# Optimization experiments

Hardware: AMD Instinct MI355X
Metric: run time of the kernel (lower is better)

The kernel has to match this reference:

```python
import jax, jax.numpy as jnp
import numpy as np

HIDDEN = 2048
NUM_INPUTS = 4
ACTIVE_IDX = 0
EPS = 1e-6


def rms_norm(x, scale, eps=EPS):
    # Gemma3n RMSNorm: compute in float32, scale by learned per-channel weight.
    x32 = x.astype(jnp.float32)
    inv = jax.lax.rsqrt(jnp.mean(x32 * x32, axis=-1, keepdims=True) + eps)
    return (x32 * inv * scale.astype(jnp.float32)).astype(x.dtype)


def compute_modalities(x, router_norm_scale, router_w):
    # router_norm -> * hidden_size**-1 -> Dense(N) -> tanh (in fp32)
    router_inputs = rms_norm(x, router_norm_scale) * (1.0 / HIDDEN)
    routed = jnp.einsum('bsh,hn->bsn', router_inputs, router_w)
    return jnp.tanh(routed.astype(jnp.float32)).astype(x.dtype)


def setup_inputs() -> dict:
    key = jax.random.key(0)
    k = jax.random.split(key, 7)
    N, B, S, H = NUM_INPUTS, 4, 2048, HIDDEN
    return {
        'hidden_states': jax.random.normal(k[0], (N, B, S, H), dtype=jnp.float32),
        'activated': jax.random.normal(k[1], (B, S, H), dtype=jnp.float32),
        'router_norm_scale': jnp.ones((H,), dtype=jnp.float32) + 0.02 * jax.random.normal(k[2], (H,), dtype=jnp.float32),
        'router_w': 0.02 * jax.random.normal(k[3], (H, N), dtype=jnp.float32),
        'pred_w': 0.02 * jax.random.normal(k[4], (N, N * N), dtype=jnp.float32),
        'corr_w': 0.02 * jax.random.normal(k[5], (N, N), dtype=jnp.float32),
        'correct_output_scale': jax.random.normal(k[6], (H,), dtype=jnp.float32),
    }


def reference(hidden_states, activated, router_norm_scale, router_w, pred_w, corr_w, correct_output_scale):
    N = NUM_INPUTS
    B, S, H = activated.shape

    # ---- predict ----
    mod_p = compute_modalities(hidden_states[ACTIVE_IDX], router_norm_scale, router_w)  # [B,S,N]
    raw = jnp.einsum('bsn,nk->bsk', mod_p, pred_w).reshape(B, S, N, N)  # [B,S,N,N]
    # keras: transpose(raw,(0,1,3,2)) then matmul(hs^(1,2,3,0), .) then transpose back
    # predictions[m,b,s,h] = sum_n hs[n,b,s,h] * raw[b,s,m,n]
    predictions = jnp.einsum('nbsh,bsmn->mbsh', hidden_states, raw) + hidden_states

    # ---- correct ----
    mod_c = compute_modalities(activated, router_norm_scale, router_w)  # [B,S,N]
    innovation = activated - predictions[ACTIVE_IDX]  # [B,S,H]
    coefs = jnp.einsum('bsn,nm->bsm', mod_c, corr_w) + 1.0  # [B,S,N]
    corrected = predictions + innovation[None] * jnp.transpose(coefs, (2, 0, 1))[..., None]

    # ---- scale_corrected_output ----
    return corrected * correct_output_scale
```

## Files before the change

### kernel.cpp

```cpp
#include <hip/hip_runtime.h>

#define HID 2048
#define NTHREADS 256

typedef float f32x4 __attribute__((ext_vector_type(4)));

__global__ __launch_bounds__(NTHREADS) void altup_fused(
    const float* __restrict__ hs,
    const float* __restrict__ act,
    const float* __restrict__ rns,
    const float* __restrict__ rw,
    const float* __restrict__ pw,
    const float* __restrict__ cw,
    const float* __restrict__ cscale,
    float* __restrict__ out,
    int T)
{
    const int t   = blockIdx.x;
    const int tid = threadIdx.x;
    const int c0  = tid * 4;
    const int c1  = c0 + 1024;

    __shared__ float s_red[4][10];

    const size_t tok     = (size_t)t * HID;
    const size_t strideN = (size_t)T * HID;

    float x0a[4], x0b[4], aa[4], ab[4], nsa[4], nsb[4], wa[16], wb[16];
    *(f32x4*)x0a = *(const f32x4*)(hs  + tok + c0);
    *(f32x4*)x0b = *(const f32x4*)(hs  + tok + c1);
    *(f32x4*)aa  = *(const f32x4*)(act + tok + c0);
    *(f32x4*)ab  = *(const f32x4*)(act + tok + c1);
    *(f32x4*)nsa = *(const f32x4*)(rns + c0);
    *(f32x4*)nsb = *(const f32x4*)(rns + c1);
    #pragma unroll
    for (int r = 0; r < 4; ++r) {
        *(f32x4*)(wa + 4 * r) = *(const f32x4*)(rw + (size_t)(c0 + r) * 4);
        *(f32x4*)(wb + 4 * r) = *(const f32x4*)(rw + (size_t)(c1 + r) * 4);
    }

    float red[10];
    #pragma unroll
    for (int k = 0; k < 10; ++k) red[k] = 0.f;
    #pragma unroll
    for (int j = 0; j < 4; ++j) {
        float x0 = x0a[j], a = aa[j], ns = nsa[j];
        red[0] += x0 * x0;
        red[1] += a * a;
        float xs = x0 * ns, as_ = a * ns;
        #pragma unroll
        for (int n = 0; n < 4; ++n) {
            red[2 + n] += xs  * wa[4 * j + n];
            red[6 + n] += as_ * wa[4 * j + n];
        }
    }
    #pragma unroll
    for (int j = 0; j < 4; ++j) {
        float x0 = x0b[j], a = ab[j], ns = nsb[j];
        red[0] += x0 * x0;
        red[1] += a * a;
        float xs = x0 * ns, as_ = a * ns;
        #pragma unroll
        for (int n = 0; n < 4; ++n) {
            red[2 + n] += xs  * wb[4 * j + n];
            red[6 + n] += as_ * wb[4 * j + n];
        }
    }

    float x1a[4], x1b[4], x2a[4], x2b[4], x3a[4], x3b[4], csa[4], csb[4];
    *(f32x4*)x1a = *(const f32x4*)(hs + 1 * strideN + tok + c0);
    *(f32x4*)x1b = *(const f32x4*)(hs + 1 * strideN + tok + c1);
    *(f32x4*)x2a = *(const f32x4*)(hs + 2 * strideN + tok + c0);
    *(f32x4*)x2b = *(const f32x4*)(hs + 2 * strideN + tok + c1);
    *(f32x4*)x3a = *(const f32x4*)(hs + 3 * strideN + tok + c0);
    *(f32x4*)x3b = *(const f32x4*)(hs + 3 * strideN + tok + c1);
    *(f32x4*)csa = *(const f32x4*)(cscale + c0);
    *(f32x4*)csb = *(const f32x4*)(cscale + c1);

    #pragma unroll
    for (int off = 32; off > 0; off >>= 1) {
        #pragma unroll
        for (int k = 0; k < 10; ++k) red[k] += __shfl_down(red[k], off, 64);
    }
    const int wave = tid >> 6, lane = tid & 63;
    if (lane == 0) {
        #pragma unroll
        for (int k = 0; k < 10; ++k) s_red[wave][k] = red[k];
    }
    __syncthreads();

    float acc[10];
    #pragma unroll
    for (int k = 0; k < 10; ++k)
        acc[k] = s_red[0][k] + s_red[1][k] + s_red[2][k] + s_red[3][k];

    const float invH  = 1.0f / (float)HID;
    const float inv_p = rsqrtf(acc[0] * invH + 1e-6f) * invH;
    const float inv_c = rsqrtf(acc[1] * invH + 1e-6f) * invH;
    float mp[4], mc[4];
    #pragma unroll
    for (int n = 0; n < 4; ++n) {
        mp[n] = tanhf(acc[2 + n] * inv_p);
        mc[n] = tanhf(acc[6 + n] * inv_c);
    }
    float raw[16];
    #pragma unroll
    for (int kk = 0; kk < 16; ++kk)
        raw[kk] = mp[0] * pw[kk]      + mp[1] * pw[16 + kk]
                + mp[2] * pw[32 + kk] + mp[3] * pw[48 + kk];
    float coef[4];
    #pragma unroll
    for (int m = 0; m < 4; ++m)
        coef[m] = 1.0f + mc[0] * cw[m]     + mc[1] * cw[4 + m]
                       + mc[2] * cw[8 + m] + mc[3] * cw[12 + m];

    auto emit = [&](const float* x0, const float* x1, const float* x2,
                    const float* x3, const float* a, const float* cs,
                    size_t off) {
        float o[4][4];
        #pragma unroll
        for (int j = 0; j < 4; ++j) {
            float x[4] = { x0[j], x1[j], x2[j], x3[j] };
            float pred[4];
            #pragma unroll
            for (int m = 0; m < 4; ++m)
                pred[m] = x[0] * raw[4 * m + 0] + x[1] * raw[4 * m + 1]
                        + x[2] * raw[4 * m + 2] + x[3] * raw[4 * m + 3] + x[m];
            float innov = a[j] - pred[0];
            #pragma unroll
            for (int m = 0; m < 4; ++m)
                o[m][j] = (pred[m] + innov * coef[m]) * cs[j];
        }
        #pragma unroll
        for (int m = 0; m < 4; ++m)
            __builtin_nontemporal_store(*(const f32x4*)o[m],
                                        (f32x4*)(out + (size_t)m * strideN + off));
    };
    emit(x0a, x1a, x2a, x3a, aa, csa, tok + c0);
    emit(x0b, x1b, x2b, x3b, ab, csb, tok + c1);
}

extern "C" void kernel_launch(void* const* d_in, const int* in_sizes, int n_in,
                              void* d_out, int out_size, void* d_ws, size_t ws_size,
                              hipStream_t stream) {
    const float* hs  = (const float*)d_in[0];
    const float* act = (const float*)d_in[1];
    const float* rns = (const float*)d_in[2];
    const float* rw  = (const float*)d_in[3];
    const float* pw  = (const float*)d_in[4];
    const float* cw  = (const float*)d_in[5];
    const float* cs  = (const float*)d_in[6];
    float* out = (float*)d_out;

    const int T = in_sizes[1] / HID;
    altup_fused<<<dim3(T), dim3(NTHREADS), 0, stream>>>(hs, act, rns, rw, pw, cw, cs, out, T);
}
```

Before: 492.0 us.

## Assign one token per wavefront and drop block-level shared-memory reduction

Each 64-lane wave now processes a whole token (8 chunks of 256 columns), so the reduction is done purely with xor-shuffles and the shared-memory staging and __syncthreads are gone. The grid shrinks by four because each block handles four tokens. The second pass reloads hidden_states slot 0 and the activated row from memory (likely L2) instead of keeping them in registers, which trades extra cache traffic for lower register pressure and no block barrier.

```diff
diff --git a/kernel.cpp b/kernel.cpp
--- a/kernel.cpp
+++ b/kernel.cpp
@@ -16,92 +16,58 @@
     float* __restrict__ out,
     int T)
 {
-    const int t   = blockIdx.x;
-    const int tid = threadIdx.x;
-    const int c0  = tid * 4;
-    const int c1  = c0 + 1024;
-
-    __shared__ float s_red[4][10];
+    const int wave = threadIdx.x >> 6;
+    const int lane = threadIdx.x & 63;
+    const int t    = blockIdx.x * 4 + wave;
+    if (t >= T) return;
 
     const size_t tok     = (size_t)t * HID;
     const size_t strideN = (size_t)T * HID;
-
-    float x0a[4], x0b[4], aa[4], ab[4], nsa[4], nsb[4], wa[16], wb[16];
-    *(f32x4*)x0a = *(const f32x4*)(hs  + tok + c0);
-    *(f32x4*)x0b = *(const f32x4*)(hs  + tok + c1);
-    *(f32x4*)aa  = *(const f32x4*)(act + tok + c0);
-    *(f32x4*)ab  = *(const f32x4*)(act + tok + c1);
-    *(f32x4*)nsa = *(const f32x4*)(rns + c0);
-    *(f32x4*)nsb = *(const f32x4*)(rns + c1);
-    #pragma unroll
-    for (int r = 0; r < 4; ++r) {
-        *(f32x4*)(wa + 4 * r) = *(const f32x4*)(rw + (size_t)(c0 + r) * 4);
-        *(f32x4*)(wb + 4 * r) = *(const f32x4*)(rw + (size_t)(c1 + r) * 4);
-    }
+    const int    l4      = lane * 4;
 
     float red[10];
     #pragma unroll
     for (int k = 0; k < 10; ++k) red[k] = 0.f;
+
     #pragma unroll
-    for (int j = 0; j < 4; ++j) {
-        float x0 = x0a[j], a = aa[j], ns = nsa[j];
-        red[0] += x0 * x0;
-        red[1] += a * a;
-        float xs = x0 * ns, as_ = a * ns;
+    for (int c = 0; c < 8; ++c) {
+        const int off = c * 256 + l4;
+        float x0[4], a[4], ns[4], w[16];
+        *(f32x4*)x0 = *(const f32x4*)(hs  + tok + off);
+        *(f32x4*)a  = *(const f32x4*)(act + tok + off);
+        *(f32x4*)ns = *(const f32x4*)(rns + off);
         #pragma unroll
-        for (int n = 0; n < 4; ++n) {
-            red[2 + n] += xs  * wa[4 * j + n];
-            red[6 + n] += as_ * wa[4 * j + n];
-        }
-    }
-    #pragma unroll
-    for (int j = 0; j < 4; ++j) {
-        float x0 = x0b[j], a = ab[j], ns = nsb[j];
-        red[0] += x0 * x0;
-        red[1] += a * a;
-        float xs = x0 * ns, as_ = a * ns;
+        for (int r = 0; r < 4; ++r)
+            *(f32x4*)(w + 4 * r) = *(const f32x4*)(rw + (size_t)(off + r) * 4);
         #pragma unroll
-        for (int n = 0; n < 4; ++n) {
-            red[2 + n] += xs  * wb[4 * j + n];
-            red[6 + n] += as_ * wb[4 * j + n];
+        for (int j = 0; j < 4; ++j) {
+            float xv = x0[j], av = a[j], nv = ns[j];
+            red[0] += xv * xv;
+            red[1] += av * av;
+            float xs = xv * nv, as_ = av * nv;
+            #pragma unroll
+            for (int n = 0; n < 4; ++n) {
+                red[2 + n] += xs  * w[4 * j + n];
+                red[6 + n] += as_ * w[4 * j + n];
+            }
         }
     }
 
-    float x1a[4], x1b[4], x2a[4], x2b[4], x3a[4], x3b[4], csa[4], csb[4];
-    *(f32x4*)x1a = *(const f32x4*)(hs + 1 * strideN + tok + c0);
-    *(f32x4*)x1b = *(const f32x4*)(hs + 1 * strideN + tok + c1);
-    *(f32x4*)x2a = *(const f32x4*)(hs + 2 * strideN + tok + c0);
-    *(f32x4*)x2b = *(const f32x4*)(hs + 2 * strideN + tok + c1);
-    *(f32x4*)x3a = *(const f32x4*)(hs + 3 * strideN + tok + c0);
-    *(f32x4*)x3b = *(const f32x4*)(hs + 3 * strideN + tok + c1);
-    *(f32x4*)csa = *(const f32x4*)(cscale + c0);
-    *(f32x4*)csb = *(const f32x4*)(cscale + c1);
-
     #pragma unroll
-    for (int off = 32; off > 0; off >>= 1) {
+    for (int m = 32; m > 0; m >>= 1) {
         #pragma unroll
-        for (int k = 0; k < 10; ++k) red[k] += __shfl_down(red[k], off, 64);
+        for (int k = 0; k < 10; ++k)
+            red[k] += __shfl_xor(red[k], m, 64);
     }
-    const int wave = tid >> 6, lane = tid & 63;
-    if (lane == 0) {
-        #pragma unroll
-        for (int k = 0; k < 10; ++k) s_red[wave][k] = red[k];
-    }
-    __syncthreads();
-
-    float acc[10];
-    #pragma unroll
-    for (int k = 0; k < 10; ++k)
-        acc[k] = s_red[0][k] + s_red[1][k] + s_red[2][k] + s_red[3][k];
 
     const float invH  = 1.0f / (float)HID;
-    const float inv_p = rsqrtf(acc[0] * invH + 1e-6f) * invH;
-    const float inv_c = rsqrtf(acc[1] * invH + 1e-6f) * invH;
+    const float inv_p = rsqrtf(red[0] * invH + 1e-6f) * invH;
+    const float inv_c = rsqrtf(red[1] * invH + 1e-6f) * invH;
     float mp[4], mc[4];
     #pragma unroll
     for (int n = 0; n < 4; ++n) {
-        mp[n] = tanhf(acc[2 + n] * inv_p);
-        mc[n] = tanhf(acc[6 + n] * inv_c);
+        mp[n] = tanhf(red[2 + n] * inv_p);
+        mc[n] = tanhf(red[6 + n] * inv_c);
     }
     float raw[16];
     #pragma unroll
@@ -114,9 +80,17 @@
         coef[m] = 1.0f + mc[0] * cw[m]     + mc[1] * cw[4 + m]
                        + mc[2] * cw[8 + m] + mc[3] * cw[12 + m];
 
-    auto emit = [&](const float* x0, const float* x1, const float* x2,
-                    const float* x3, const float* a, const float* cs,
-                    size_t off) {
+    #pragma unroll
+    for (int c = 0; c < 8; ++c) {
+        const int off = c * 256 + l4;
+        float x0[4], x1[4], x2[4], x3[4], a[4], cs[4];
+        *(f32x4*)x0 = *(const f32x4*)(hs + 0 * strideN + tok + off);
+        *(f32x4*)x1 = *(const f32x4*)(hs + 1 * strideN + tok + off);
+        *(f32x4*)x2 = *(const f32x4*)(hs + 2 * strideN + tok + off);
+        *(f32x4*)x3 = *(const f32x4*)(hs + 3 * strideN + tok + off);
+        *(f32x4*)a  = *(const f32x4*)(act + tok + off);
+        *(f32x4*)cs = *(const f32x4*)(cscale + off);
+
         float o[4][4];
         #pragma unroll
         for (int j = 0; j < 4; ++j) {
@@ -134,10 +108,8 @@
         #pragma unroll
         for (int m = 0; m < 4; ++m)
             __builtin_nontemporal_store(*(const f32x4*)o[m],
-                                        (f32x4*)(out + (size_t)m * strideN + off));
-    };
-    emit(x0a, x1a, x2a, x3a, aa, csa, tok + c0);
-    emit(x0b, x1b, x2b, x3b, ab, csb, tok + c1);
+                (f32x4*)(out + (size_t)m * strideN + tok + off));
+    }
 }
 
 extern "C" void kernel_launch(void* const* d_in, const int* in_sizes, int n_in,
@@ -153,5 +125,6 @@
     float* out = (float*)d_out;
 
     const int T = in_sizes[1] / HID;
-    altup_fused<<<dim3(T), dim3(NTHREADS), 0, stream>>>(hs, act, rns, rw, pw, cw, cs, out, T);
+    altup_fused<<<dim3((T + 3) / 4), dim3(NTHREADS), 0, stream>>>(
+        hs, act, rns, rw, pw, cw, cs, out, T);
 }
```

Result: slower. 518.0 us (+5.3%).
